# Optimization experiments

Measured on AMD Instinct MI355X. Metric: run time of the kernel, lower is better.

## Reference

```python
import jax, jax.numpy as jnp
import numpy as np

NEG_SLOPE = 0.2  # PyG GATv2Conv default


def _glorot(key, shape):
    fan_in, fan_out = shape[0], shape[1]
    lim = (6.0 / (fan_in + fan_out)) ** 0.5
    return jax.random.uniform(key, shape, jnp.float32, -lim, lim)


def setup_inputs() -> dict:
    key = jax.random.key(0)
    ks = jax.random.split(key, 20)
    N, E = 30000, 480000
    IN, HID, H, OUT = 16, 64, 4, 2
    d1 = HID * H  # 256
    inp = {
        "x": jax.random.normal(ks[0], (N, IN), jnp.float32),
        "edge_index": jax.random.randint(ks[1], (2, E), 0, N, jnp.int64),
        # conv1: in=16 -> heads=4, out=64, concat
        "Wl1": _glorot(ks[2], (IN, d1)), "bl1": jnp.zeros((d1,), jnp.float32),
        "Wr1": _glorot(ks[3], (IN, d1)), "br1": jnp.zeros((d1,), jnp.float32),
        "att1": _glorot(ks[4], (H, HID)), "b1": jnp.zeros((d1,), jnp.float32),
        # conv2: 256 -> heads=4, out=64, concat
        "Wl2": _glorot(ks[5], (d1, d1)), "bl2": jnp.zeros((d1,), jnp.float32),
        "Wr2": _glorot(ks[6], (d1, d1)), "br2": jnp.zeros((d1,), jnp.float32),
        "att2": _glorot(ks[7], (H, HID)), "b2": jnp.zeros((d1,), jnp.float32),
        # conv3: 256 -> heads=1, out=64, mean (concat=False)
        "Wl3": _glorot(ks[8], (d1, HID)), "bl3": jnp.zeros((HID,), jnp.float32),
        "Wr3": _glorot(ks[9], (d1, HID)), "br3": jnp.zeros((HID,), jnp.float32),
        "att3": _glorot(ks[10], (1, HID)), "b3": jnp.zeros((HID,), jnp.float32),
        # fc: 64 -> 2
        "Wfc": _glorot(ks[11], (HID, OUT)), "bfc": jnp.zeros((OUT,), jnp.float32),
    }
    return inp


def _gatv2(x, Wl, bl, Wr, br, att, b, src, dst, n_nodes, concat):
    """One GATv2Conv layer (PyG semantics, share_weights=False, eval mode)."""
    H, C = att.shape
    xl = (x @ Wl + bl).reshape(-1, H, C)  # source projection [N,H,C]
    xr = (x @ Wr + br).reshape(-1, H, C)  # target projection [N,H,C]
    # per-edge attention logit: a^T leaky_relu(xl_j + xr_i)
    e = jax.nn.leaky_relu(xl[src] + xr[dst], NEG_SLOPE)          # [E,H,C]
    score = jnp.einsum('ehc,hc->eh', e, att)                     # [E,H]
    # segment softmax over edges sharing the same destination node
    m = jax.ops.segment_max(score, dst, num_segments=n_nodes)    # [N,H]
    p = jnp.exp(score - m[dst])
    s = jax.ops.segment_sum(p, dst, num_segments=n_nodes)        # [N,H]
    alpha = p / (s[dst] + 1e-16)                                 # [E,H]
    out = jax.ops.segment_sum(alpha[:, :, None] * xl[src], dst,
                              num_segments=n_nodes)              # [N,H,C]
    out = out.reshape(n_nodes, H * C) if concat else out.mean(axis=1)
    return out + b


def reference(x, edge_index, Wl1, bl1, Wr1, br1, att1, b1,
              Wl2, bl2, Wr2, br2, att2, b2,
              Wl3, bl3, Wr3, br3, att3, b3, Wfc, bfc):
    n = x.shape[0]
    # PyG GATv2Conv adds self-loops by default
    loops = jnp.arange(n, dtype=edge_index.dtype)
    src = jnp.concatenate([edge_index[0], loops])
    dst = jnp.concatenate([edge_index[1], loops])
    # dropout(p=0.6) is identity in eval mode
    h = jax.nn.elu(_gatv2(x, Wl1, bl1, Wr1, br1, att1, b1, src, dst, n, True))
    h = jax.nn.elu(_gatv2(h, Wl2, bl2, Wr2, br2, att2, b2, src, dst, n, True))
    h = _gatv2(h, Wl3, bl3, Wr3, br3, att3, b3, src, dst, n, False)
    return h @ Wfc + bfc
```

## Files before the change

kernel.cpp:

```cpp
#include <hip/hip_runtime.h>
#include <math.h>

typedef __attribute__((ext_vector_type(8))) short bf16x8;
typedef __attribute__((ext_vector_type(4))) float f32x4;
typedef __attribute__((ext_vector_type(2))) float f32x2;

__device__ inline unsigned short f2bf(float f) {
    union { float f; unsigned u; } v; v.f = f;
    unsigned r = v.u + 0x7FFFu + ((v.u >> 16) & 1u);
    return (unsigned short)(r >> 16);
}
__device__ inline float bf2f(unsigned short s) {
    union { unsigned u; float f; } v; v.u = ((unsigned)s) << 16;
    return v.f;
}

__device__ inline void wconv_elem(const float* __restrict__ W,
                                  unsigned short* __restrict__ Bh,
                                  unsigned short* __restrict__ Bl,
                                  int idx, int NC) {
    int k = idx / NC, n = idx - k * NC;
    float f = W[idx];
    unsigned short h = f2bf(f);
    Bh[n * 256 + k] = h;
    Bl[n * 256 + k] = f2bf(f - bf2f(h));
}

__global__ __launch_bounds__(256) void k_prep(int* __restrict__ deg, int N,
                                              const float* __restrict__ Wl2,
                                              const float* __restrict__ Wr2,
                                              const float* __restrict__ Wl3,
                                              const float* __restrict__ Wr3,
                                              unsigned short* __restrict__ W2lh,
                                              unsigned short* __restrict__ W2ll,
                                              unsigned short* __restrict__ W2rh,
                                              unsigned short* __restrict__ W2rl,
                                              unsigned short* __restrict__ W3lh,
                                              unsigned short* __restrict__ W3ll,
                                              unsigned short* __restrict__ W3rh,
                                              unsigned short* __restrict__ W3rl) {
    int idx = blockIdx.x * 256 + threadIdx.x;
    if (idx < N) { deg[idx] = 1; return; }
    idx -= N;
    if (idx < 65536) { wconv_elem(Wl2, W2lh, W2ll, idx, 256); return; }
    idx -= 65536;
    if (idx < 65536) { wconv_elem(Wr2, W2rh, W2rl, idx, 256); return; }
    idx -= 65536;
    if (idx < 16384) { wconv_elem(Wl3, W3lh, W3ll, idx, 64); return; }
    idx -= 16384;
    if (idx < 16384) { wconv_elem(Wr3, W3rh, W3rl, idx, 64); }
}

__global__ __launch_bounds__(256) void k_count(const int* __restrict__ dst, int E,
                                               int* __restrict__ deg) {
    int e = blockIdx.x * 256 + threadIdx.x;
    if (e < E) atomicAdd(&deg[dst[e]], 1);
}

__global__ __launch_bounds__(1024) void k_scan1(const int* __restrict__ deg,
                                                int* __restrict__ excl,
                                                int* __restrict__ bsum, int N) {
    __shared__ int wsum[17];
    int t = threadIdx.x, lane = t & 63, wid = t >> 6;
    int idx = blockIdx.x * 1024 + t;
    int v = (idx < N) ? deg[idx] : 0;
    int x = v;
    #pragma unroll
    for (int off = 1; off < 64; off <<= 1) {
        int y = __shfl_up(x, off, 64);
        if (lane >= off) x += y;
    }
    if (lane == 63) wsum[wid] = x;
    __syncthreads();
    if (wid == 0 && lane < 16) {
        int w = wsum[lane];
        int xs = w;
        #pragma unroll
        for (int off = 1; off < 16; off <<= 1) {
            int y = __shfl_up(xs, off, 64);
            if (lane >= off) xs += y;
        }
        wsum[lane] = xs - w;
        if (lane == 15) wsum[16] = xs;
    }
    __syncthreads();
    int incl = x + wsum[wid];
    if (idx < N) excl[idx] = incl - v;
    if (t == 0) bsum[blockIdx.x] = wsum[16];
}

__global__ __launch_bounds__(1024) void k_scan23(const int* __restrict__ excl,
                                                 const int* __restrict__ bsum,
                                                 int* __restrict__ rowptr,
                                                 int* __restrict__ cursor, int N, int nb) {
    __shared__ int s_off, s_tot;
    int t = threadIdx.x;
    if (t < 64) {
        int v = (t < nb) ? bsum[t] : 0;
        int x = v;
        #pragma unroll
        for (int off = 1; off < 64; off <<= 1) {
            int y = __shfl_up(x, off, 64);
            if (t >= off) x += y;
        }
        if (t == (int)blockIdx.x) s_off = x - v;
        if (t == 63) s_tot = x;
    }
    __syncthreads();
    int idx = blockIdx.x * 1024 + t;
    if (idx < N) {
        int e = excl[idx] + s_off;
        rowptr[idx] = e;
        cursor[idx] = e;
    }
    if (idx == 0) rowptr[N] = s_tot;
}

__global__ __launch_bounds__(256) void k_scatter(const int* __restrict__ src,
                                                 const int* __restrict__ dst,
                                                 int E, int N,
                                                 int* __restrict__ cursor,
                                                 int* __restrict__ col) {
    int idx = blockIdx.x * 256 + threadIdx.x;
    if (idx < E) {
        int d = dst[idx];
        int pos = atomicAdd(&cursor[d], 1);
        col[pos] = src[idx];
    } else if (idx < E + N) {
        int i = idx - E;
        int pos = atomicAdd(&cursor[i], 1);
        col[pos] = i;
    } else if (idx < E + N + 64) {
        col[idx] = 0;
    }
}

__global__ __launch_bounds__(256) void gemm_bias2(const float* __restrict__ A,
                                                  const float* __restrict__ W1,
                                                  const float* __restrict__ b1,
                                                  const float* __restrict__ W2,
                                                  const float* __restrict__ b2,
                                                  unsigned short* __restrict__ C1b,
                                                  float* __restrict__ C2,
                                                  int M, int K, int NC) {
    __shared__ float As[16][68];
    __shared__ float Bs[2][16][68];
    int tid = threadIdx.x;
    int tx = tid & 15, ty = tid >> 4;
    int m0 = blockIdx.y * 64, n0 = blockIdx.x * 64;
    float acc[2][4][4] = {};
    for (int k0 = 0; k0 < K; k0 += 16) {
        #pragma unroll
        for (int i = 0; i < 4; ++i) {
            int idx = tid + i * 256;
            int r = idx >> 4, c = idx & 15;
            int row = m0 + r;
            As[c][r] = (row < M) ? A[(size_t)row * K + k0 + c] : 0.f;
        }
        #pragma unroll
        for (int i = 0; i < 4; ++i) {
            int idx = tid + i * 256;
            int r = idx >> 6, c = idx & 63;
            Bs[0][r][c] = W1[(size_t)(k0 + r) * NC + n0 + c];
            Bs[1][r][c] = W2[(size_t)(k0 + r) * NC + n0 + c];
        }
        __syncthreads();
        #pragma unroll
        for (int k = 0; k < 16; ++k) {
            float a[4], b[4], b2v[4];
            #pragma unroll
            for (int i = 0; i < 4; ++i) a[i] = As[k][ty * 4 + i];
            #pragma unroll
            for (int i = 0; i < 4; ++i) b[i] = Bs[0][k][tx * 4 + i];
            #pragma unroll
            for (int i = 0; i < 4; ++i) b2v[i] = Bs[1][k][tx * 4 + i];
            #pragma unroll
            for (int i = 0; i < 4; ++i)
                #pragma unroll
                for (int j = 0; j < 4; ++j) {
                    acc[0][i][j] += a[i] * b[j];
                    acc[1][i][j] += a[i] * b2v[j];
                }
        }
        __syncthreads();
    }
    #pragma unroll
    for (int i = 0; i < 4; ++i) {
        int row = m0 + ty * 4 + i;
        if (row < M) {
            #pragma unroll
            for (int j = 0; j < 4; ++j) {
                int cn = n0 + tx * 4 + j;
                C1b[(size_t)row * NC + cn] = f2bf(acc[0][i][j] + b1[cn]);
                C2[(size_t)row * NC + cn] = acc[1][i][j] + b2[cn];
            }
        }
    }
}

#define LDA 40

template<int NF>
__global__ __launch_bounds__(512) void gemm_dual(const unsigned short* __restrict__ Ahg,
                                                 const unsigned short* __restrict__ Alg,
                                                 const unsigned short* __restrict__ B1hg,
                                                 const unsigned short* __restrict__ B1lg,
                                                 const unsigned short* __restrict__ B2hg,
                                                 const unsigned short* __restrict__ B2lg,
                                                 const float* __restrict__ bias1,
                                                 const float* __restrict__ bias2,
                                                 unsigned short* __restrict__ C1b,
                                                 float* __restrict__ C2,
                                                 int M, int NC) {
    const int KD = 256;
    const int BN = NF * 64;
    __shared__ unsigned short Ah[128 * LDA], Al[128 * LDA];
    __shared__ unsigned short Bs[4][BN * LDA];

    int tid = threadIdx.x;
    int lane = tid & 63;
    int wid = tid >> 6;
    int m0 = blockIdx.y * 128;
    int n0 = blockIdx.x * BN;
    int wm = (wid >> 2) * 64;
    int wn = (wid & 3) * (NF * 16);
    int r16 = lane & 15;
    int g8 = (lane >> 4) * 8;
    int g = lane >> 4;

    int srow = tid >> 2;
    int schunk = (tid & 3) * 8;
    int arow_g = m0 + srow;
    if (arow_g >= M) arow_g = M - 1;
    const unsigned short* gAh = Ahg + (size_t)arow_g * KD + schunk;
    const unsigned short* gAl = Alg + (size_t)arow_g * KD + schunk;
    bool bact = (NF == 2) || (tid < 256);
    int bcol = (NF == 2) ? srow : (tid >> 2);
    size_t boff = (size_t)(n0 + (bcol < BN ? bcol : 0)) * KD + schunk;
    const unsigned short* gB[4] = { B1hg + boff, B1lg + boff, B2hg + boff, B2lg + boff };

    f32x4 acc[2][4][NF];
    #pragma unroll
    for (int o = 0; o < 2; ++o)
        #pragma unroll
        for (int mf = 0; mf < 4; ++mf)
            #pragma unroll
            for (int nf = 0; nf < NF; ++nf)
                #pragma unroll
                for (int q = 0; q < 4; ++q) acc[o][mf][nf][q] = 0.f;

    bf16x8 sa_h = *(const bf16x8*)gAh;
    bf16x8 sa_l = *(const bf16x8*)gAl;
    bf16x8 sb0, sb1, sb2, sb3;
    if (bact) {
        sb0 = *(const bf16x8*)gB[0];
        sb1 = *(const bf16x8*)gB[1];
        sb2 = *(const bf16x8*)gB[2];
        sb3 = *(const bf16x8*)gB[3];
    }

    for (int k = 0; k < 8; ++k) {
        __syncthreads();
        *(bf16x8*)&Ah[srow * LDA + schunk] = sa_h;
        *(bf16x8*)&Al[srow * LDA + schunk] = sa_l;
        if (bact) {
            *(bf16x8*)&Bs[0][bcol * LDA + schunk] = sb0;
            *(bf16x8*)&Bs[1][bcol * LDA + schunk] = sb1;
            *(bf16x8*)&Bs[2][bcol * LDA + schunk] = sb2;
            *(bf16x8*)&Bs[3][bcol * LDA + schunk] = sb3;
        }
        __syncthreads();
        if (k < 7) {
            int k0n = (k + 1) * 32;
            sa_h = *(const bf16x8*)(gAh + k0n);
            sa_l = *(const bf16x8*)(gAl + k0n);
            if (bact) {
                sb0 = *(const bf16x8*)(gB[0] + k0n);
                sb1 = *(const bf16x8*)(gB[1] + k0n);
                sb2 = *(const bf16x8*)(gB[2] + k0n);
                sb3 = *(const bf16x8*)(gB[3] + k0n);
            }
        }
        bf16x8 ah[4], al[4];
        #pragma unroll
        for (int mf = 0; mf < 4; ++mf) {
            int base = (wm + mf * 16 + r16) * LDA + g8;
            ah[mf] = *(const bf16x8*)&Ah[base];
            al[mf] = *(const bf16x8*)&Al[base];
        }
        #pragma unroll
        for (int o = 0; o < 2; ++o) {
            #pragma unroll
            for (int nf = 0; nf < NF; ++nf) {
                int base = (wn + nf * 16 + r16) * LDA + g8;
                bf16x8 bh = *(const bf16x8*)&Bs[o * 2 + 0][base];
                bf16x8 bl = *(const bf16x8*)&Bs[o * 2 + 1][base];
                #pragma unroll
                for (int mf = 0; mf < 4; ++mf) {
                    acc[o][mf][nf] = __builtin_amdgcn_mfma_f32_16x16x32_bf16(ah[mf], bh, acc[o][mf][nf], 0, 0, 0);
                    acc[o][mf][nf] = __builtin_amdgcn_mfma_f32_16x16x32_bf16(ah[mf], bl, acc[o][mf][nf], 0, 0, 0);
                    acc[o][mf][nf] = __builtin_amdgcn_mfma_f32_16x16x32_bf16(al[mf], bh, acc[o][mf][nf], 0, 0, 0);
                }
            }
        }
    }

    #pragma unroll
    for (int nf = 0; nf < NF; ++nf) {
        int cn = n0 + wn + nf * 16 + r16;
        float bv1 = bias1[cn], bv2 = bias2[cn];
        #pragma unroll
        for (int mf = 0; mf < 4; ++mf) {
            #pragma unroll
            for (int r = 0; r < 4; ++r) {
                int row = m0 + wm + mf * 16 + g * 4 + r;
                if (row < M) {
                    C1b[(size_t)row * NC + cn] = f2bf(acc[0][mf][nf][r] + bv1);
                    C2[(size_t)row * NC + cn] = acc[1][mf][nf][r] + bv2;
                }
            }
        }
    }
}

__global__ __launch_bounds__(64) void gat_agg4(const unsigned short* __restrict__ xlb,
                                               const float* __restrict__ xr,
                                               const float* __restrict__ att,
                                               const float* __restrict__ bias,
                                               const int* __restrict__ rowptr,
                                               const int* __restrict__ col,
                                               unsigned short* __restrict__ Hh,
                                               unsigned short* __restrict__ Hl,
                                               int N) {
    int i = blockIdx.x;
    int lane = threadIdx.x;
    int sub = lane & 31;
    int half = lane >> 5;
    const float L2E = 1.44269504089f;
    f32x2 xr2[4], a06[4], a04[4];
    {
        float4 a = *(const float4*)(xr + (size_t)i * 256 + sub * 8);
        float4 b = *(const float4*)(xr + (size_t)i * 256 + sub * 8 + 4);
        xr2[0].x = a.x; xr2[0].y = a.y; xr2[1].x = a.z; xr2[1].y = a.w;
        xr2[2].x = b.x; xr2[2].y = b.y; xr2[3].x = b.z; xr2[3].y = b.w;
        float4 c = *(const float4*)(att + sub * 8);
        float4 d = *(const float4*)(att + sub * 8 + 4);
        float av[8] = {c.x, c.y, c.z, c.w, d.x, d.y, d.z, d.w};
        #pragma unroll
        for (int q = 0; q < 4; ++q) {
            a06[q].x = av[2 * q] * (0.6f * L2E);     a06[q].y = av[2 * q + 1] * (0.6f * L2E);
            a04[q].x = av[2 * q] * (0.4f * L2E);     a04[q].y = av[2 * q + 1] * (0.4f * L2E);
        }
    }
    int e0 = rowptr[i], e1 = rowptr[i + 1];
    int nE = e1 - e0;
    int T = (nE + 1) >> 1;
    int lim = half ? (nE - T) : T;
    int limL = lim > 0 ? lim - 1 : 0;
    const int* cb = col + e0 + (half ? T : 0);

    auto jl = [&](int t) -> int { return cb[t < limL ? t : limL]; };
    auto ld = [&](int j) -> bf16x8 {
        return *(const bf16x8*)(xlb + (size_t)j * 256 + sub * 8);
    };

    float ss = 0.f;
    f32x2 acc2[4] = {};

    #define PROC(R, IT) { \
        union { bf16x8 v; unsigned u[4]; } uu; uu.v = (R); \
        f32x2 va_[4]; \
        f32x2 s06_ = {0.f, 0.f}, s04_ = {0.f, 0.f}; \
        _Pragma("unroll") \
        for (int q = 0; q < 4; ++q) { \
            union { unsigned a; float f; } lo_, hi_; \
            lo_.a = uu.u[q] << 16; hi_.a = uu.u[q] & 0xffff0000u; \
            va_[q].x = lo_.f; va_[q].y = hi_.f; \
            f32x2 t_ = va_[q] + xr2[q]; \
            s06_ += t_ * a06[q]; \
            f32x2 ab_; \
            ab_.x = __builtin_fabsf(t_.x); ab_.y = __builtin_fabsf(t_.y); \
            s04_ += ab_ * a04[q]; \
        } \
        f32x2 sc_ = s06_ + s04_; \
        float s_ = sc_.x + sc_.y; \
        s_ += __shfl_xor(s_, 1); \
        s_ += __shfl_xor(s_, 2); \
        s_ += __shfl_xor(s_, 4); \
        bool valid_ = (IT) < lim; \
        float p_ = valid_ ? __builtin_amdgcn_exp2f(s_) : 0.f; \
        ss += p_; \
        f32x2 pp_; pp_.x = p_; pp_.y = p_; \
        _Pragma("unroll") \
        for (int q = 0; q < 4; ++q) acc2[q] += pp_ * va_[q]; \
    }

    int j0 = jl(0), j1 = jl(1), j2 = jl(2), j3 = jl(3);
    bf16x8 r0 = ld(j0), r1 = ld(j1), r2 = ld(j2), r3 = ld(j3);
    int j4 = jl(4), j5 = jl(5), j6 = jl(6), j7 = jl(7);
    bf16x8 r4 = ld(j4), r5 = ld(j5), r6 = ld(j6), r7 = ld(j7);
    j0 = jl(8); j1 = jl(9); j2 = jl(10); j3 = jl(11);

    int t = 0;
    while (t + 8 <= T) {
        PROC(r0, t + 0); PROC(r1, t + 1); PROC(r2, t + 2); PROC(r3, t + 3);
        r0 = ld(j0); r1 = ld(j1); r2 = ld(j2); r3 = ld(j3);
        j0 = jl(t + 12); j1 = jl(t + 13); j2 = jl(t + 14); j3 = jl(t + 15);
        PROC(r4, t + 4); PROC(r5, t + 5); PROC(r6, t + 6); PROC(r7, t + 7);
        r4 = ld(j0); r5 = ld(j1); r6 = ld(j2); r7 = ld(j3);
        j0 = jl(t + 16); j1 = jl(t + 17); j2 = jl(t + 18); j3 = jl(t + 19);
        t += 8;
    }
    if (t + 0 < T) PROC(r0, t + 0);
    if (t + 1 < T) PROC(r1, t + 1);
    if (t + 2 < T) PROC(r2, t + 2);
    if (t + 3 < T) PROC(r3, t + 3);
    if (t + 4 < T) PROC(r4, t + 4);
    if (t + 5 < T) PROC(r5, t + 5);
    if (t + 6 < T) PROC(r6, t + 6);
    if (t + 7 < T) PROC(r7, t + 7);
    #undef PROC

    ss += __shfl_xor(ss, 32);
    #pragma unroll
    for (int q = 0; q < 4; ++q) {
        acc2[q].x += __shfl_xor(acc2[q].x, 32);
        acc2[q].y += __shfl_xor(acc2[q].y, 32);
    }

    if (lane < 32) {
        float inv = 1.f / ss;
        float accf[8];
        #pragma unroll
        for (int q = 0; q < 4; ++q) { accf[2 * q] = acc2[q].x; accf[2 * q + 1] = acc2[q].y; }
        bf16x8 hv, lv;
        #pragma unroll
        for (int c = 0; c < 8; ++c) {
            float o = fmaf(accf[c], inv, bias[sub * 8 + c]);
            o = o > 0.f ? o : __expf(o) - 1.f;
            unsigned short h_ = f2bf(o);
            hv[c] = (short)h_;
            lv[c] = (short)f2bf(o - bf2f(h_));
        }
        *(bf16x8*)(Hh + (size_t)i * 256 + sub * 8) = hv;
        *(bf16x8*)(Hl + (size_t)i * 256 + sub * 8) = lv;
    }
}

__global__ __launch_bounds__(64) void gat_agg1_fc(const unsigned short* __restrict__ xlb,
                                                  const float* __restrict__ xr,
                                                  const float* __restrict__ att,
                                                  const float* __restrict__ bias,
                                                  const float* __restrict__ Wfc,
                                                  const float* __restrict__ bfc,
                                                  const int* __restrict__ rowptr,
                                                  const int* __restrict__ col,
                                                  float* __restrict__ out, int N) {
    int i = blockIdx.x;
    int lane = threadIdx.x;
    int sub = lane & 15;
    int qh = lane >> 4;
    const float L2E = 1.44269504089f;
    f32x2 xr2[2], a06[2], a04[2];
    {
        float4 a = *(const float4*)(xr + (size_t)i * 64 + sub * 4);
        xr2[0].x = a.x; xr2[0].y = a.y; xr2[1].x = a.z; xr2[1].y = a.w;
        float4 c = *(const float4*)(att + sub * 4);
        float av[4] = {c.x, c.y, c.z, c.w};
        #pragma unroll
        for (int q = 0; q < 2; ++q) {
            a06[q].x = av[2 * q] * (0.6f * L2E);     a06[q].y = av[2 * q + 1] * (0.6f * L2E);
            a04[q].x = av[2 * q] * (0.4f * L2E);     a04[q].y = av[2 * q + 1] * (0.4f * L2E);
        }
    }
    int e0 = rowptr[i], e1 = rowptr[i + 1];
    int nE = e1 - e0;
    int T = (nE + 3) >> 2;
    int lim = nE - qh * T;
    lim = lim < 0 ? 0 : (lim > T ? T : lim);
    int limL = lim > 0 ? lim - 1 : 0;
    const int* cb = col + e0 + qh * T;

    auto jl = [&](int t) -> int { return cb[t < limL ? t : limL]; };
    auto ld = [&](int j) -> ushort4 {
        return *(const ushort4*)(xlb + (size_t)j * 64 + sub * 4);
    };

    float ss = 0.f;
    f32x2 acc2[2] = {};

    #define PROC1(R, IT) { \
        ushort4 rr_ = (R); \
        f32x2 va_[2]; \
        { union { unsigned a; float f; } c0_, c1_, c2_, c3_; \
          c0_.a = ((unsigned)rr_.x) << 16; c1_.a = ((unsigned)rr_.y) << 16; \
          c2_.a = ((unsigned)rr_.z) << 16; c3_.a = ((unsigned)rr_.w) << 16; \
          va_[0].x = c0_.f; va_[0].y = c1_.f; va_[1].x = c2_.f; va_[1].y = c3_.f; } \
        f32x2 s06_ = {0.f, 0.f}, s04_ = {0.f, 0.f}; \
        _Pragma("unroll") \
        for (int q = 0; q < 2; ++q) { \
            f32x2 t_ = va_[q] + xr2[q]; \
            s06_ += t_ * a06[q]; \
            f32x2 ab_; \
            ab_.x = __builtin_fabsf(t_.x); ab_.y = __builtin_fabsf(t_.y); \
            s04_ += ab_ * a04[q]; \
        } \
        f32x2 sc_ = s06_ + s04_; \
        float s_ = sc_.x + sc_.y; \
        s_ += __shfl_xor(s_, 1); \
        s_ += __shfl_xor(s_, 2); \
        s_ += __shfl_xor(s_, 4); \
        s_ += __shfl_xor(s_, 8); \
        bool valid_ = (IT) < lim; \
        float p_ = valid_ ? __builtin_amdgcn_exp2f(s_) : 0.f; \
        ss += p_; \
        f32x2 pp_; pp_.x = p_; pp_.y = p_; \
        acc2[0] += pp_ * va_[0]; \
        acc2[1] += pp_ * va_[1]; \
    }

    int j0 = jl(0), j1 = jl(1), j2 = jl(2), j3 = jl(3);
    ushort4 r0 = ld(j0), r1 = ld(j1), r2 = ld(j2), r3 = ld(j3);
    int j4 = jl(4), j5 = jl(5), j6 = jl(6), j7 = jl(7);
    ushort4 r4 = ld(j4), r5 = ld(j5), r6 = ld(j6), r7 = ld(j7);
    j0 = jl(8); j1 = jl(9); j2 = jl(10); j3 = jl(11);

    int t = 0;
    while (t + 8 <= T) {
        PROC1(r0, t + 0); PROC1(r1, t + 1); PROC1(r2, t + 2); PROC1(r3, t + 3);
        r0 = ld(j0); r1 = ld(j1); r2 = ld(j2); r3 = ld(j3);
        j0 = jl(t + 12); j1 = jl(t + 13); j2 = jl(t + 14); j3 = jl(t + 15);
        PROC1(r4, t + 4); PROC1(r5, t + 5); PROC1(r6, t + 6); PROC1(r7, t + 7);
        r4 = ld(j0); r5 = ld(j1); r6 = ld(j2); r7 = ld(j3);
        j0 = jl(t + 16); j1 = jl(t + 17); j2 = jl(t + 18); j3 = jl(t + 19);
        t += 8;
    }
    if (t + 0 < T) PROC1(r0, t + 0);
    if (t + 1 < T) PROC1(r1, t + 1);
    if (t + 2 < T) PROC1(r2, t + 2);
    if (t + 3 < T) PROC1(r3, t + 3);
    if (t + 4 < T) PROC1(r4, t + 4);
    if (t + 5 < T) PROC1(r5, t + 5);
    if (t + 6 < T) PROC1(r6, t + 6);
    if (t + 7 < T) PROC1(r7, t + 7);
    #undef PROC1

    ss += __shfl_xor(ss, 16);
    ss += __shfl_xor(ss, 32);
    float accf[4] = {acc2[0].x, acc2[0].y, acc2[1].x, acc2[1].y};
    #pragma unroll
    for (int c = 0; c < 4; ++c) {
        accf[c] += __shfl_xor(accf[c], 16);
        accf[c] += __shfl_xor(accf[c], 32);
    }

    float inv = 1.f / ss;
    float q0 = 0.f, q1 = 0.f;
    #pragma unroll
    for (int c = 0; c < 4; ++c) {
        float h = fmaf(accf[c], inv, bias[sub * 4 + c]);
        q0 = fmaf(h, Wfc[(sub * 4 + c) * 2 + 0], q0);
        q1 = fmaf(h, Wfc[(sub * 4 + c) * 2 + 1], q1);
    }
    q0 += __shfl_xor(q0, 1); q1 += __shfl_xor(q1, 1);
    q0 += __shfl_xor(q0, 2); q1 += __shfl_xor(q1, 2);
    q0 += __shfl_xor(q0, 4); q1 += __shfl_xor(q1, 4);
    q0 += __shfl_xor(q0, 8); q1 += __shfl_xor(q1, 8);
    if (lane == 0) {
        out[(size_t)i * 2 + 0] = q0 + bfc[0];
        out[(size_t)i * 2 + 1] = q1 + bfc[1];
    }
}

extern "C" void kernel_launch(void* const* d_in, const int* in_sizes, int n_in,
                              void* d_out, int out_size, void* d_ws, size_t ws_size,
                              hipStream_t stream) {
    const float* x    = (const float*)d_in[0];
    const int*   ei   = (const int*)d_in[1];
    const float* Wl1  = (const float*)d_in[2];
    const float* bl1  = (const float*)d_in[3];
    const float* Wr1  = (const float*)d_in[4];
    const float* br1  = (const float*)d_in[5];
    const float* att1 = (const float*)d_in[6];
    const float* b1   = (const float*)d_in[7];
    const float* Wl2  = (const float*)d_in[8];
    const float* bl2  = (const float*)d_in[9];
    const float* Wr2  = (const float*)d_in[10];
    const float* br2  = (const float*)d_in[11];
    const float* att2 = (const float*)d_in[12];
    const float* b2   = (const float*)d_in[13];
    const float* Wl3  = (const float*)d_in[14];
    const float* bl3  = (const float*)d_in[15];
    const float* Wr3  = (const float*)d_in[16];
    const float* br3  = (const float*)d_in[17];
    const float* att3 = (const float*)d_in[18];
    const float* b3   = (const float*)d_in[19];
    const float* Wfc  = (const float*)d_in[20];
    const float* bfc  = (const float*)d_in[21];
    float* out = (float*)d_out;

    const int N = in_sizes[0] / 16;
    const int E = in_sizes[1] / 2;
    const int* srcp = ei;
    const int* dstp = ei + E;

    char* ws = (char*)d_ws;
    size_t off = 0;
    auto take = [&](size_t bytes) -> char* {
        char* p = ws + off;
        off = (off + bytes + 255) & ~(size_t)255;
        return p;
    };
    const int nb = (N + 1023) / 1024;
    int* rowptr = (int*)take((size_t)(N + 1) * 4);
    int* cursor = (int*)take((size_t)N * 4);
    int* deg    = (int*)take((size_t)N * 4);
    int* excl   = (int*)take((size_t)N * 4);
    int* bsum   = (int*)take((size_t)(nb + 1) * 4);
    int* col    = (int*)take((size_t)(E + N + 64) * 4);
    unsigned short* xlb = (unsigned short*)take((size_t)N * 256 * 2);
    float* xr   = (float*)take((size_t)N * 256 * 4);
    unsigned short* Hh = (unsigned short*)take((size_t)N * 256 * 2);
    unsigned short* Hl = (unsigned short*)take((size_t)N * 256 * 2);
    unsigned short* W2lh = (unsigned short*)take(256 * 256 * 2);
    unsigned short* W2ll = (unsigned short*)take(256 * 256 * 2);
    unsigned short* W2rh = (unsigned short*)take(256 * 256 * 2);
    unsigned short* W2rl = (unsigned short*)take(256 * 256 * 2);
    unsigned short* W3lh = (unsigned short*)take(256 * 64 * 2);
    unsigned short* W3ll = (unsigned short*)take(256 * 64 * 2);
    unsigned short* W3rh = (unsigned short*)take(256 * 64 * 2);
    unsigned short* W3rl = (unsigned short*)take(256 * 64 * 2);
    (void)ws_size; (void)n_in; (void)out_size;

    {
        int total = N + 65536 + 65536 + 16384 + 16384;
        k_prep<<<dim3((total + 255) / 256), dim3(256), 0, stream>>>(
            deg, N, Wl2, Wr2, Wl3, Wr3,
            W2lh, W2ll, W2rh, W2rl, W3lh, W3ll, W3rh, W3rl);
    }
    k_count<<<dim3((E + 255) / 256), dim3(256), 0, stream>>>(dstp, E, deg);
    k_scan1<<<dim3(nb), dim3(1024), 0, stream>>>(deg, excl, bsum, N);
    k_scan23<<<dim3(nb), dim3(1024), 0, stream>>>(excl, bsum, rowptr, cursor, N, nb);
    k_scatter<<<dim3((E + N + 64 + 255) / 256), dim3(256), 0, stream>>>(srcp, dstp, E, N, cursor, col);

    dim3 agg_grid(N);
    int mblk = (N + 127) / 128;

    gemm_bias2<<<dim3(4, (N + 63) / 64), dim3(256), 0, stream>>>(
        x, Wl1, bl1, Wr1, br1, xlb, xr, N, 16, 256);
    gat_agg4<<<agg_grid, dim3(64), 0, stream>>>(xlb, xr, att1, b1, rowptr, col, Hh, Hl, N);

    gemm_dual<2><<<dim3(2, mblk), dim3(512), 0, stream>>>(
        Hh, Hl, W2lh, W2ll, W2rh, W2rl, bl2, br2, xlb, xr, N, 256);
    gat_agg4<<<agg_grid, dim3(64), 0, stream>>>(xlb, xr, att2, b2, rowptr, col, Hh, Hl, N);

    gemm_dual<1><<<dim3(1, mblk), dim3(512), 0, stream>>>(
        Hh, Hl, W3lh, W3ll, W3rh, W3rl, bl3, br3, xlb, xr, N, 64);
    gat_agg1_fc<<<agg_grid, dim3(64), 0, stream>>>(xlb, xr, att3, b3, Wfc, bfc, rowptr, col, out, N);
}
```

Baseline: 242.9 us.

## Split 4-head aggregation across two wavefronts and fold degree count into prep

The 4-head aggregation kernel now runs 128 threads per node, giving four edge streams instead of two, and combines the partial sums of the second wave through shared memory. This targets the latency-bound per-node gather by adding more loads in flight. The degree count is merged into the weight-conversion prep kernel, the self-loop +1 moves into the scan, and a memset replaces the deg init. The cost is an extra barrier and shared-memory reduction per node, plus idle lanes on nodes with few edges.

```diff
diff --git a/kernel.cpp b/kernel.cpp
--- a/kernel.cpp
+++ b/kernel.cpp
@@ -26,7 +26,8 @@
     Bl[n * 256 + k] = f2bf(f - bf2f(h));
 }
 
-__global__ __launch_bounds__(256) void k_prep(int* __restrict__ deg, int N,
+__global__ __launch_bounds__(256) void k_prep(const int* __restrict__ dst, int E,
+                                              int* __restrict__ deg,
                                               const float* __restrict__ Wl2,
                                               const float* __restrict__ Wr2,
                                               const float* __restrict__ Wl3,
@@ -40,21 +41,15 @@
                                               unsigned short* __restrict__ W3rh,
                                               unsigned short* __restrict__ W3rl) {
     int idx = blockIdx.x * 256 + threadIdx.x;
-    if (idx < N) { deg[idx] = 1; return; }
-    idx -= N;
     if (idx < 65536) { wconv_elem(Wl2, W2lh, W2ll, idx, 256); return; }
     idx -= 65536;
     if (idx < 65536) { wconv_elem(Wr2, W2rh, W2rl, idx, 256); return; }
     idx -= 65536;
     if (idx < 16384) { wconv_elem(Wl3, W3lh, W3ll, idx, 64); return; }
     idx -= 16384;
-    if (idx < 16384) { wconv_elem(Wr3, W3rh, W3rl, idx, 64); }
-}
-
-__global__ __launch_bounds__(256) void k_count(const int* __restrict__ dst, int E,
-                                               int* __restrict__ deg) {
-    int e = blockIdx.x * 256 + threadIdx.x;
-    if (e < E) atomicAdd(&deg[dst[e]], 1);
+    if (idx < 16384) { wconv_elem(Wr3, W3rh, W3rl, idx, 64); return; }
+    idx -= 16384;
+    if (idx < E) atomicAdd(&deg[dst[idx]], 1);
 }
 
 __global__ __launch_bounds__(1024) void k_scan1(const int* __restrict__ deg,
@@ -63,7 +58,7 @@
     __shared__ int wsum[17];
     int t = threadIdx.x, lane = t & 63, wid = t >> 6;
     int idx = blockIdx.x * 1024 + t;
-    int v = (idx < N) ? deg[idx] : 0;
+    int v = (idx < N) ? deg[idx] + 1 : 0;
     int x = v;
     #pragma unroll
     for (int off = 1; off < 64; off <<= 1) {
@@ -323,19 +318,23 @@
     }
 }
 
-__global__ __launch_bounds__(64) void gat_agg4(const unsigned short* __restrict__ xlb,
-                                               const float* __restrict__ xr,
-                                               const float* __restrict__ att,
-                                               const float* __restrict__ bias,
-                                               const int* __restrict__ rowptr,
-                                               const int* __restrict__ col,
-                                               unsigned short* __restrict__ Hh,
-                                               unsigned short* __restrict__ Hl,
-                                               int N) {
+__global__ __launch_bounds__(128) void gat_agg4(const unsigned short* __restrict__ xlb,
+                                                const float* __restrict__ xr,
+                                                const float* __restrict__ att,
+                                                const float* __restrict__ bias,
+                                                const int* __restrict__ rowptr,
+                                                const int* __restrict__ col,
+                                                unsigned short* __restrict__ Hh,
+                                                unsigned short* __restrict__ Hl,
+                                                int N) {
+    __shared__ float red[32][12];
     int i = blockIdx.x;
-    int lane = threadIdx.x;
+    int tid = threadIdx.x;
+    int lane = tid & 63;
+    int wid = tid >> 6;
     int sub = lane & 31;
     int half = lane >> 5;
+    int strm = wid * 2 + half;
     const float L2E = 1.44269504089f;
     f32x2 xr2[4], a06[4], a04[4];
     {
@@ -354,10 +353,11 @@
     }
     int e0 = rowptr[i], e1 = rowptr[i + 1];
     int nE = e1 - e0;
-    int T = (nE + 1) >> 1;
-    int lim = half ? (nE - T) : T;
+    int T = (nE + 3) >> 2;
+    int lim = nE - strm * T;
+    lim = lim < 0 ? 0 : (lim > T ? T : lim);
     int limL = lim > 0 ? lim - 1 : 0;
-    const int* cb = col + e0 + (half ? T : 0);
+    const int* cb = col + e0 + strm * T;
 
     auto jl = [&](int t) -> int { return cb[t < limL ? t : limL]; };
     auto ld = [&](int j) -> bf16x8 {
@@ -428,7 +428,22 @@
         acc2[q].y += __shfl_xor(acc2[q].y, 32);
     }
 
-    if (lane < 32) {
+    if (wid == 1 && lane < 32) {
+        #pragma unroll
+        for (int q = 0; q < 4; ++q) {
+            red[sub][2 * q] = acc2[q].x;
+            red[sub][2 * q + 1] = acc2[q].y;
+        }
+        red[sub][8] = ss;
+    }
+    __syncthreads();
+    if (wid == 0 && lane < 32) {
+        #pragma unroll
+        for (int q = 0; q < 4; ++q) {
+            acc2[q].x += red[sub][2 * q];
+            acc2[q].y += red[sub][2 * q + 1];
+        }
+        ss += red[sub][8];
         float inv = 1.f / ss;
         float accf[8];
         #pragma unroll
@@ -632,13 +647,13 @@
     unsigned short* W3rl = (unsigned short*)take(256 * 64 * 2);
     (void)ws_size; (void)n_in; (void)out_size;
 
+    hipMemsetAsync(deg, 0, (size_t)N * 4, stream);
     {
-        int total = N + 65536 + 65536 + 16384 + 16384;
+        int total = 65536 + 65536 + 16384 + 16384 + E;
         k_prep<<<dim3((total + 255) / 256), dim3(256), 0, stream>>>(
-            deg, N, Wl2, Wr2, Wl3, Wr3,
+            dstp, E, deg, Wl2, Wr2, Wl3, Wr3,
             W2lh, W2ll, W2rh, W2rl, W3lh, W3ll, W3rh, W3rl);
     }
-    k_count<<<dim3((E + 255) / 256), dim3(256), 0, stream>>>(dstp, E, deg);
     k_scan1<<<dim3(nb), dim3(1024), 0, stream>>>(deg, excl, bsum, N);
     k_scan23<<<dim3(nb), dim3(1024), 0, stream>>>(excl, bsum, rowptr, cursor, N, nb);
     k_scatter<<<dim3((E + N + 64 + 255) / 256), dim3(256), 0, stream>>>(srcp, dstp, E, N, cursor, col);
@@ -648,11 +663,11 @@
 
     gemm_bias2<<<dim3(4, (N + 63) / 64), dim3(256), 0, stream>>>(
         x, Wl1, bl1, Wr1, br1, xlb, xr, N, 16, 256);
-    gat_agg4<<<agg_grid, dim3(64), 0, stream>>>(xlb, xr, att1, b1, rowptr, col, Hh, Hl, N);
+    gat_agg4<<<agg_grid, dim3(128), 0, stream>>>(xlb, xr, att1, b1, rowptr, col, Hh, Hl, N);
 
     gemm_dual<2><<<dim3(2, mblk), dim3(512), 0, stream>>>(
         Hh, Hl, W2lh, W2ll, W2rh, W2rl, bl2, br2, xlb, xr, N, 256);
-    gat_agg4<<<agg_grid, dim3(64), 0, stream>>>(xlb, xr, att2, b2, rowptr, col, Hh, Hl, N);
+    gat_agg4<<<agg_grid, dim3(128), 0, stream>>>(xlb, xr, att2, b2, rowptr, col, Hh, Hl, N);
 
     gemm_dual<1><<<dim3(1, mblk), dim3(512), 0, stream>>>(
         Hh, Hl, W3lh, W3ll, W3rh, W3rl, bl3, br3, xlb, xr, N, 64);
```

After: 268.9 us. 10.7% more time.
